# Optimization experiments

Measured on AMD Instinct MI355X. Metric: run time of the kernel, lower is better.

The kernel has to match this reference:

```python
import jax, jax.numpy as jnp
import numpy as np

K = 512        # num_embeddings
D = 64         # embedding_dim
BETA = 0.25
B, S = 64, 4096


def setup_inputs() -> dict:
    key = jax.random.key(0)
    k1, k2 = jax.random.split(key)
    latents = jax.random.normal(k1, (B, S, D), dtype=jnp.float32)
    # torch init: uniform_(-1/K, 1/K)
    embedding = jax.random.uniform(k2, (K, D), dtype=jnp.float32,
                                   minval=-1.0 / K, maxval=1.0 / K)
    return {"latents": latents, "embedding": embedding}


def reference(latents, embedding):
    d = embedding.shape[1]
    flat = latents.reshape(-1, d)                       # [N, D]
    # squared-euclidean distances via norm expansion: [N, K]
    dist = (jnp.sum(flat * flat, axis=1, keepdims=True)
            + jnp.sum(embedding * embedding, axis=1)
            - 2.0 * flat @ embedding.T)
    inds = jnp.argmin(dist, axis=1)                     # [N] (channel = identity)
    # one-hot @ codebook == gather; same math, no [N,K] one-hot materialized
    quantized = embedding[inds].reshape(latents.shape)  # [B, S, D]
    commitment_loss = jnp.mean((jax.lax.stop_gradient(quantized) - latents) ** 2)
    embedding_loss = jnp.mean((quantized - jax.lax.stop_gradient(latents)) ** 2)
    vq_loss = commitment_loss * BETA + embedding_loss
    # straight-through estimator
    quantized_st = latents + jax.lax.stop_gradient(quantized - latents)
    return quantized_st, vq_loss
```

## Files before the change

kernel.cpp:

```cpp
#include <hip/hip_runtime.h>
#include <math.h>
#include <stdint.h>

#define KCODES 512
#define DIM 64
#define NROWS (64 * 4096)
#define BLOCK 512
#define ROWS_PER_WAVE 16
#define BM ((BLOCK / 64) * ROWS_PER_WAVE)
#define NBLK (NROWS / BM)

typedef float f32x4 __attribute__((ext_vector_type(4)));
typedef long long i64t;

typedef __attribute__((address_space(3))) uint32_t* lds_ptr_t;
typedef const __attribute__((address_space(1))) uint32_t* glb_ptr_t;

__global__ void vq_prep_kernel(const float* __restrict__ emb,
                               float* __restrict__ en512,
                               uint8_t* __restrict__ ebf8) {
    int k = blockIdx.x * blockDim.x + threadIdx.x;
    if (k >= KCODES) return;
    const float4* e4 = reinterpret_cast<const float4*>(emb + k * DIM);
    float s0 = 0.f, s1 = 0.f, s2 = 0.f, s3 = 0.f;
#pragma unroll
    for (int j = 0; j < 8; ++j) {
        float4 v0 = e4[j * 2];
        float4 v1 = e4[j * 2 + 1];
        s0 = fmaf(v0.x, v0.x, s0); s1 = fmaf(v0.y, v0.y, s1);
        s2 = fmaf(v0.z, v0.z, s2); s3 = fmaf(v0.w, v0.w, s3);
        s0 = fmaf(v1.x, v1.x, s0); s1 = fmaf(v1.y, v1.y, s1);
        s2 = fmaf(v1.z, v1.z, s2); s3 = fmaf(v1.w, v1.w, s3);
        uint32_t lo = 0, hi = 0;
        lo = __builtin_amdgcn_cvt_pk_fp8_f32(-1024.f * v0.x, -1024.f * v0.y, lo, false);
        lo = __builtin_amdgcn_cvt_pk_fp8_f32(-1024.f * v0.z, -1024.f * v0.w, lo, true);
        hi = __builtin_amdgcn_cvt_pk_fp8_f32(-1024.f * v1.x, -1024.f * v1.y, hi, false);
        hi = __builtin_amdgcn_cvt_pk_fp8_f32(-1024.f * v1.z, -1024.f * v1.w, hi, true);
        uint2 p; p.x = lo; p.y = hi;
        *reinterpret_cast<uint2*>(&ebf8[k * DIM + ((j ^ (k & 7)) << 3)]) = p;
    }
    en512[k] = 512.f * (1.0f + (s0 + s1) + (s2 + s3));
}

__launch_bounds__(BLOCK, 8)
__global__ void vq_mfma_kernel(const float* __restrict__ lat,
                               const float* __restrict__ emb,
                               const float* __restrict__ en512,
                               const uint8_t* __restrict__ ebf8,
                               float* __restrict__ outq,
                               float* __restrict__ partials) {
    __shared__ __align__(16) uint8_t e_lds[KCODES * DIM];
    __shared__ float en_lds[KCODES];
    __shared__ float wsum_lds[BLOCK / 64];

    const int t = threadIdx.x;
    const int lane = t & 63, wid = t >> 6;
    const int l15 = lane & 15, lq = lane >> 4;
    const int swz = l15 & 7;

    const uint32_t bid = (blockIdx.x & 7) * (NBLK / 8) + (blockIdx.x >> 3);
    const uint32_t waverow = bid * BM + (uint32_t)wid * ROWS_PER_WAVE;

#pragma unroll
    for (int i = 0; i < 4; ++i) {
        int c = t + i * BLOCK;
        __builtin_amdgcn_global_load_lds(
            (glb_ptr_t)(const void*)(ebf8 + c * 16),
            (lds_ptr_t)(void*)(&e_lds[c * 16]), 16, 0, 0);
    }

    float4 araw[2][2];
#pragma unroll
    for (int ks = 0; ks < 2; ++ks) {
        const float* xp = lat + (waverow + l15) * DIM + ks * 32 + lq * 8;
        araw[ks][0] = reinterpret_cast<const float4*>(xp)[0];
        araw[ks][1] = reinterpret_cast<const float4*>(xp)[1];
    }
    en_lds[t] = en512[t];
    __syncthreads();

    float xsq = 0.f, lsum = 0.f;
    i64t afrag[2];
#pragma unroll
    for (int ks = 0; ks < 2; ++ks) {
        float4 v0 = araw[ks][0], v1 = araw[ks][1];
        xsq = fmaf(v0.x, v0.x, xsq); xsq = fmaf(v0.y, v0.y, xsq);
        xsq = fmaf(v0.z, v0.z, xsq); xsq = fmaf(v0.w, v0.w, xsq);
        xsq = fmaf(v1.x, v1.x, xsq); xsq = fmaf(v1.y, v1.y, xsq);
        xsq = fmaf(v1.z, v1.z, xsq); xsq = fmaf(v1.w, v1.w, xsq);
        uint32_t lo = 0, hi = 0;
        lo = __builtin_amdgcn_cvt_pk_fp8_f32(v0.x, v0.y, lo, false);
        lo = __builtin_amdgcn_cvt_pk_fp8_f32(v0.z, v0.w, lo, true);
        hi = __builtin_amdgcn_cvt_pk_fp8_f32(v1.x, v1.y, hi, false);
        hi = __builtin_amdgcn_cvt_pk_fp8_f32(v1.z, v1.w, hi, true);
        afrag[ks] = (i64t)(((uint64_t)hi << 32) | (uint64_t)lo);
    }

    uint32_t best[4];
#pragma unroll
    for (int r = 0; r < 4; ++r) best[r] = 0xFFFFFFFFu;

#pragma unroll 4
    for (int nf = 0; nf < 32; ++nf) {
        const int n = nf * 16 + l15;
        i64t b0 = *reinterpret_cast<const i64t*>(
            &e_lds[n * DIM + ((lq ^ swz) << 3)]);
        i64t b1 = *reinterpret_cast<const i64t*>(
            &e_lds[n * DIM + (((lq + 4) ^ swz) << 3)]);
        float en = en_lds[n];
        f32x4 acc = {en, en, en, en};
        acc = __builtin_amdgcn_mfma_f32_16x16x32_fp8_fp8(afrag[0], b0, acc, 0, 0, 0);
        acc = __builtin_amdgcn_mfma_f32_16x16x32_fp8_fp8(afrag[1], b1, acc, 0, 0, 0);
        const uint32_t nn = (uint32_t)n;
#pragma unroll
        for (int r = 0; r < 4; ++r) {
            uint32_t k = (__float_as_uint(acc[r]) & 0xFFFFFE00u) | nn;
            best[r] = min(best[r], k);
        }
    }

#pragma unroll
    for (int off = 1; off < 16; off <<= 1) {
#pragma unroll
        for (int r = 0; r < 4; ++r) {
            uint32_t o = (uint32_t)__shfl_xor((int)best[r], off, 64);
            best[r] = min(best[r], o);
        }
    }

    if (l15 == 0) {
#pragma unroll
        for (int r = 0; r < 4; ++r)
            lsum = fmaf(__uint_as_float(best[r] & 0xFFFFFE00u),
                        (1.f / 512.f), lsum - 1.0f);
    }

    const float4* emb4 = reinterpret_cast<const float4*>(emb);
    float4* out4 = reinterpret_cast<float4*>(outq);
#pragma unroll
    for (int r = 0; r < 4; ++r) {
        const uint32_t k = best[r] & 511u;
        const uint32_t grow = waverow + lq * 4 + r;
        float4 e4 = emb4[k * 16 + l15];
        out4[grow * 16 + l15] = e4;
    }

    lsum += xsq;

#pragma unroll
    for (int off = 32; off > 0; off >>= 1)
        lsum += __shfl_down(lsum, off, 64);
    if (lane == 0) wsum_lds[wid] = lsum;
    __syncthreads();
    if (t == 0) {
        float s = 0.f;
#pragma unroll
        for (int w = 0; w < BLOCK / 64; ++w) s += wsum_lds[w];
        partials[blockIdx.x] = s;
    }
}

__global__ void vq_loss_kernel(const float* __restrict__ partials,
                               float* __restrict__ loss) {
    float s = 0.f;
    for (int i = threadIdx.x; i < NBLK; i += 256) s += partials[i];
#pragma unroll
    for (int off = 32; off > 0; off >>= 1)
        s += __shfl_down(s, off, 64);
    __shared__ float wsum[4];
    const int lane = threadIdx.x & 63;
    const int wid = threadIdx.x >> 6;
    if (lane == 0) wsum[wid] = s;
    __syncthreads();
    if (threadIdx.x == 0) {
        float tsum = 0.f;
#pragma unroll
        for (int w = 0; w < 4; ++w) tsum += wsum[w];
        loss[0] = 1.25f * (tsum / (float)((size_t)NROWS * DIM));
    }
}

extern "C" void kernel_launch(void* const* d_in, const int* in_sizes, int n_in,
                              void* d_out, int out_size, void* d_ws, size_t ws_size,
                              hipStream_t stream) {
    const float* lat = (const float*)d_in[0];
    const float* emb = (const float*)d_in[1];
    float* outq = (float*)d_out;
    float* loss = (float*)d_out + (size_t)NROWS * DIM;

    float* en512 = (float*)d_ws;
    uint8_t* ebf8 = (uint8_t*)d_ws + 2048;
    float* partials = (float*)((char*)d_ws + 34816);

    vq_prep_kernel<<<2, 256, 0, stream>>>(emb, en512, ebf8);
    vq_mfma_kernel<<<NBLK, BLOCK, 0, stream>>>(lat, emb, en512, ebf8, outq, partials);
    vq_loss_kernel<<<1, 256, 0, stream>>>(partials, loss);
}
```

Baseline: 41.03 us.

## Process two row chunks per block, prefetching the next chunk's latents during scoring

Each block now handles two consecutive 128-row chunks. It issues the second chunk's latent loads right after converting the first chunk, so the global load overlaps the MFMA scoring loop. This also halves the grid and amortises the 32KB codebook LDS fill over twice the rows. Latent loads and quantized stores now use nontemporal hints. The costs are fewer blocks to hide latency and more registers held across the scoring loop.

```diff
diff --git a/kernel.cpp b/kernel.cpp
--- a/kernel.cpp
+++ b/kernel.cpp
@@ -8,7 +8,8 @@
 #define BLOCK 512
 #define ROWS_PER_WAVE 16
 #define BM ((BLOCK / 64) * ROWS_PER_WAVE)
-#define NBLK (NROWS / BM)
+#define CHUNKS 2
+#define NBLK (NROWS / (BM * CHUNKS))
 
 typedef float f32x4 __attribute__((ext_vector_type(4)));
 typedef long long i64t;
@@ -59,7 +60,7 @@
     const int swz = l15 & 7;
 
     const uint32_t bid = (blockIdx.x & 7) * (NBLK / 8) + (blockIdx.x >> 3);
-    const uint32_t waverow = bid * BM + (uint32_t)wid * ROWS_PER_WAVE;
+    const uint32_t blockrow = bid * (BM * CHUNKS);
 
 #pragma unroll
     for (int i = 0; i < 4; ++i) {
@@ -69,81 +70,103 @@
             (lds_ptr_t)(void*)(&e_lds[c * 16]), 16, 0, 0);
     }
 
-    float4 araw[2][2];
-#pragma unroll
-    for (int ks = 0; ks < 2; ++ks) {
-        const float* xp = lat + (waverow + l15) * DIM + ks * 32 + lq * 8;
-        araw[ks][0] = reinterpret_cast<const float4*>(xp)[0];
-        araw[ks][1] = reinterpret_cast<const float4*>(xp)[1];
-    }
+    f32x4 araw[2][2];
+    auto load_a = [&](int c) {
+        const uint32_t rowbase = blockrow + (uint32_t)c * BM +
+                                 (uint32_t)wid * ROWS_PER_WAVE;
+#pragma unroll
+        for (int ks = 0; ks < 2; ++ks) {
+            const float* xp = lat + (rowbase + l15) * DIM + ks * 32 + lq * 8;
+            araw[ks][0] = __builtin_nontemporal_load(
+                reinterpret_cast<const f32x4*>(xp));
+            araw[ks][1] = __builtin_nontemporal_load(
+                reinterpret_cast<const f32x4*>(xp) + 1);
+        }
+    };
+
+    load_a(0);
     en_lds[t] = en512[t];
     __syncthreads();
 
     float xsq = 0.f, lsum = 0.f;
     i64t afrag[2];
-#pragma unroll
-    for (int ks = 0; ks < 2; ++ks) {
-        float4 v0 = araw[ks][0], v1 = araw[ks][1];
-        xsq = fmaf(v0.x, v0.x, xsq); xsq = fmaf(v0.y, v0.y, xsq);
-        xsq = fmaf(v0.z, v0.z, xsq); xsq = fmaf(v0.w, v0.w, xsq);
-        xsq = fmaf(v1.x, v1.x, xsq); xsq = fmaf(v1.y, v1.y, xsq);
-        xsq = fmaf(v1.z, v1.z, xsq); xsq = fmaf(v1.w, v1.w, xsq);
-        uint32_t lo = 0, hi = 0;
-        lo = __builtin_amdgcn_cvt_pk_fp8_f32(v0.x, v0.y, lo, false);
-        lo = __builtin_amdgcn_cvt_pk_fp8_f32(v0.z, v0.w, lo, true);
-        hi = __builtin_amdgcn_cvt_pk_fp8_f32(v1.x, v1.y, hi, false);
-        hi = __builtin_amdgcn_cvt_pk_fp8_f32(v1.z, v1.w, hi, true);
-        afrag[ks] = (i64t)(((uint64_t)hi << 32) | (uint64_t)lo);
-    }
-
     uint32_t best[4];
-#pragma unroll
-    for (int r = 0; r < 4; ++r) best[r] = 0xFFFFFFFFu;
-
+
+    auto cvt_a = [&]() {
+#pragma unroll
+        for (int ks = 0; ks < 2; ++ks) {
+            f32x4 v0 = araw[ks][0], v1 = araw[ks][1];
+            xsq = fmaf(v0[0], v0[0], xsq); xsq = fmaf(v0[1], v0[1], xsq);
+            xsq = fmaf(v0[2], v0[2], xsq); xsq = fmaf(v0[3], v0[3], xsq);
+            xsq = fmaf(v1[0], v1[0], xsq); xsq = fmaf(v1[1], v1[1], xsq);
+            xsq = fmaf(v1[2], v1[2], xsq); xsq = fmaf(v1[3], v1[3], xsq);
+            uint32_t lo = 0, hi = 0;
+            lo = __builtin_amdgcn_cvt_pk_fp8_f32(v0[0], v0[1], lo, false);
+            lo = __builtin_amdgcn_cvt_pk_fp8_f32(v0[2], v0[3], lo, true);
+            hi = __builtin_amdgcn_cvt_pk_fp8_f32(v1[0], v1[1], hi, false);
+            hi = __builtin_amdgcn_cvt_pk_fp8_f32(v1[2], v1[3], hi, true);
+            afrag[ks] = (i64t)(((uint64_t)hi << 32) | (uint64_t)lo);
+        }
+    };
+
+    auto score = [&]() {
+#pragma unroll
+        for (int r = 0; r < 4; ++r) best[r] = 0xFFFFFFFFu;
 #pragma unroll 4
-    for (int nf = 0; nf < 32; ++nf) {
-        const int n = nf * 16 + l15;
-        i64t b0 = *reinterpret_cast<const i64t*>(
-            &e_lds[n * DIM + ((lq ^ swz) << 3)]);
-        i64t b1 = *reinterpret_cast<const i64t*>(
-            &e_lds[n * DIM + (((lq + 4) ^ swz) << 3)]);
-        float en = en_lds[n];
-        f32x4 acc = {en, en, en, en};
-        acc = __builtin_amdgcn_mfma_f32_16x16x32_fp8_fp8(afrag[0], b0, acc, 0, 0, 0);
-        acc = __builtin_amdgcn_mfma_f32_16x16x32_fp8_fp8(afrag[1], b1, acc, 0, 0, 0);
-        const uint32_t nn = (uint32_t)n;
+        for (int nf = 0; nf < 32; ++nf) {
+            const int n = nf * 16 + l15;
+            i64t b0 = *reinterpret_cast<const i64t*>(
+                &e_lds[n * DIM + ((lq ^ swz) << 3)]);
+            i64t b1 = *reinterpret_cast<const i64t*>(
+                &e_lds[n * DIM + (((lq + 4) ^ swz) << 3)]);
+            float en = en_lds[n];
+            f32x4 acc = {en, en, en, en};
+            acc = __builtin_amdgcn_mfma_f32_16x16x32_fp8_fp8(afrag[0], b0, acc, 0, 0, 0);
+            acc = __builtin_amdgcn_mfma_f32_16x16x32_fp8_fp8(afrag[1], b1, acc, 0, 0, 0);
+            const uint32_t nn = (uint32_t)n;
+#pragma unroll
+            for (int r = 0; r < 4; ++r) {
+                uint32_t k = (__float_as_uint(acc[r]) & 0xFFFFFE00u) | nn;
+                best[r] = min(best[r], k);
+            }
+        }
+    };
+
+    auto finish = [&](int c) {
+#pragma unroll
+        for (int off = 1; off < 16; off <<= 1) {
+#pragma unroll
+            for (int r = 0; r < 4; ++r) {
+                uint32_t o = (uint32_t)__shfl_xor((int)best[r], off, 64);
+                best[r] = min(best[r], o);
+            }
+        }
+        if (l15 == 0) {
+#pragma unroll
+            for (int r = 0; r < 4; ++r)
+                lsum = fmaf(__uint_as_float(best[r] & 0xFFFFFE00u),
+                            (1.f / 512.f), lsum - 1.0f);
+        }
+        const uint32_t rowbase = blockrow + (uint32_t)c * BM +
+                                 (uint32_t)wid * ROWS_PER_WAVE;
+        const f32x4* emb4 = reinterpret_cast<const f32x4*>(emb);
+        f32x4* out4 = reinterpret_cast<f32x4*>(outq);
 #pragma unroll
         for (int r = 0; r < 4; ++r) {
-            uint32_t k = (__float_as_uint(acc[r]) & 0xFFFFFE00u) | nn;
-            best[r] = min(best[r], k);
-        }
-    }
-
-#pragma unroll
-    for (int off = 1; off < 16; off <<= 1) {
-#pragma unroll
-        for (int r = 0; r < 4; ++r) {
-            uint32_t o = (uint32_t)__shfl_xor((int)best[r], off, 64);
-            best[r] = min(best[r], o);
-        }
-    }
-
-    if (l15 == 0) {
-#pragma unroll
-        for (int r = 0; r < 4; ++r)
-            lsum = fmaf(__uint_as_float(best[r] & 0xFFFFFE00u),
-                        (1.f / 512.f), lsum - 1.0f);
-    }
-
-    const float4* emb4 = reinterpret_cast<const float4*>(emb);
-    float4* out4 = reinterpret_cast<float4*>(outq);
-#pragma unroll
-    for (int r = 0; r < 4; ++r) {
-        const uint32_t k = best[r] & 511u;
-        const uint32_t grow = waverow + lq * 4 + r;
-        float4 e4 = emb4[k * 16 + l15];
-        out4[grow * 16 + l15] = e4;
-    }
+            const uint32_t k = best[r] & 511u;
+            const uint32_t grow = rowbase + lq * 4 + r;
+            f32x4 e4 = emb4[k * 16 + l15];
+            __builtin_nontemporal_store(e4, &out4[grow * 16 + l15]);
+        }
+    };
+
+    cvt_a();
+    load_a(1);
+    score();
+    finish(0);
+    cvt_a();
+    score();
+    finish(1);
 
     lsum += xsq;
 
```

Measured after the change: 55.24 us. 34.6% more time.

## Hold FP8 codebook in registers and stream latent rows per persistent wave

Applied to the files above, without the earlier changes.

The fused distance/argmin kernel becomes a persistent-style kernel with 512 blocks of 256 threads. Each wave loads the whole FP8 codebook into registers once as MFMA A operands, then loops over 128 latent rows with double-buffered global loads, treating the latents as the B operand. This removes the per-block LDS codebook copy and the per-fragment LDS reads. Argmin now keeps per-lane packed keys and needs only two cross-lane shuffles. The cost is very high register pressure (64 i64 codebook fragments per lane) and much lower occupancy, which may limit how well memory latency is hidden.

```diff
diff --git a/kernel.cpp b/kernel.cpp
--- a/kernel.cpp
+++ b/kernel.cpp
@@ -5,16 +5,12 @@
 #define KCODES 512
 #define DIM 64
 #define NROWS (64 * 4096)
-#define BLOCK 512
-#define ROWS_PER_WAVE 16
-#define BM ((BLOCK / 64) * ROWS_PER_WAVE)
-#define NBLK (NROWS / BM)
+#define BLOCK 256
+#define NBLK 512
+#define ROWS_PER_WAVE 128
 
 typedef float f32x4 __attribute__((ext_vector_type(4)));
 typedef long long i64t;
-
-typedef __attribute__((address_space(3))) uint32_t* lds_ptr_t;
-typedef const __attribute__((address_space(1))) uint32_t* glb_ptr_t;
 
 __global__ void vq_prep_kernel(const float* __restrict__ emb,
                                float* __restrict__ en512,
@@ -37,112 +33,119 @@
         hi = __builtin_amdgcn_cvt_pk_fp8_f32(-1024.f * v1.x, -1024.f * v1.y, hi, false);
         hi = __builtin_amdgcn_cvt_pk_fp8_f32(-1024.f * v1.z, -1024.f * v1.w, hi, true);
         uint2 p; p.x = lo; p.y = hi;
-        *reinterpret_cast<uint2*>(&ebf8[k * DIM + ((j ^ (k & 7)) << 3)]) = p;
+        *reinterpret_cast<uint2*>(&ebf8[k * DIM + (j << 3)]) = p;
     }
     en512[k] = 512.f * (1.0f + (s0 + s1) + (s2 + s3));
 }
 
-__launch_bounds__(BLOCK, 8)
-__global__ void vq_mfma_kernel(const float* __restrict__ lat,
-                               const float* __restrict__ emb,
-                               const float* __restrict__ en512,
-                               const uint8_t* __restrict__ ebf8,
-                               float* __restrict__ outq,
-                               float* __restrict__ partials) {
-    __shared__ __align__(16) uint8_t e_lds[KCODES * DIM];
+__launch_bounds__(BLOCK, 2)
+__global__ void vq_stream_kernel(const float* __restrict__ lat,
+                                 const float* __restrict__ emb,
+                                 const float* __restrict__ en512,
+                                 const uint8_t* __restrict__ ebf8,
+                                 float* __restrict__ outq,
+                                 float* __restrict__ partials) {
     __shared__ float en_lds[KCODES];
     __shared__ float wsum_lds[BLOCK / 64];
 
     const int t = threadIdx.x;
     const int lane = t & 63, wid = t >> 6;
     const int l15 = lane & 15, lq = lane >> 4;
-    const int swz = l15 & 7;
-
-    const uint32_t bid = (blockIdx.x & 7) * (NBLK / 8) + (blockIdx.x >> 3);
-    const uint32_t waverow = bid * BM + (uint32_t)wid * ROWS_PER_WAVE;
-
-#pragma unroll
-    for (int i = 0; i < 4; ++i) {
-        int c = t + i * BLOCK;
-        __builtin_amdgcn_global_load_lds(
-            (glb_ptr_t)(const void*)(ebf8 + c * 16),
-            (lds_ptr_t)(void*)(&e_lds[c * 16]), 16, 0, 0);
-    }
-
-    float4 araw[2][2];
-#pragma unroll
-    for (int ks = 0; ks < 2; ++ks) {
-        const float* xp = lat + (waverow + l15) * DIM + ks * 32 + lq * 8;
-        araw[ks][0] = reinterpret_cast<const float4*>(xp)[0];
-        araw[ks][1] = reinterpret_cast<const float4*>(xp)[1];
-    }
+    const uint32_t wrow = ((uint32_t)blockIdx.x * (BLOCK / 64) + wid) * ROWS_PER_WAVE;
+
     en_lds[t] = en512[t];
+    en_lds[t + BLOCK] = en512[t + BLOCK];
+
+    i64t acode[32][2];
+#pragma unroll
+    for (int nf = 0; nf < 32; ++nf) {
+#pragma unroll
+        for (int ks = 0; ks < 2; ++ks) {
+            acode[nf][ks] = *reinterpret_cast<const i64t*>(
+                ebf8 + (uint32_t)(nf * 16 + l15) * DIM + ks * 32 + lq * 8);
+        }
+    }
     __syncthreads();
 
     float xsq = 0.f, lsum = 0.f;
-    i64t afrag[2];
-#pragma unroll
-    for (int ks = 0; ks < 2; ++ks) {
-        float4 v0 = araw[ks][0], v1 = araw[ks][1];
-        xsq = fmaf(v0.x, v0.x, xsq); xsq = fmaf(v0.y, v0.y, xsq);
-        xsq = fmaf(v0.z, v0.z, xsq); xsq = fmaf(v0.w, v0.w, xsq);
-        xsq = fmaf(v1.x, v1.x, xsq); xsq = fmaf(v1.y, v1.y, xsq);
-        xsq = fmaf(v1.z, v1.z, xsq); xsq = fmaf(v1.w, v1.w, xsq);
-        uint32_t lo = 0, hi = 0;
-        lo = __builtin_amdgcn_cvt_pk_fp8_f32(v0.x, v0.y, lo, false);
-        lo = __builtin_amdgcn_cvt_pk_fp8_f32(v0.z, v0.w, lo, true);
-        hi = __builtin_amdgcn_cvt_pk_fp8_f32(v1.x, v1.y, hi, false);
-        hi = __builtin_amdgcn_cvt_pk_fp8_f32(v1.z, v1.w, hi, true);
-        afrag[ks] = (i64t)(((uint64_t)hi << 32) | (uint64_t)lo);
-    }
-
-    uint32_t best[4];
-#pragma unroll
-    for (int r = 0; r < 4; ++r) best[r] = 0xFFFFFFFFu;
-
-#pragma unroll 4
-    for (int nf = 0; nf < 32; ++nf) {
-        const int n = nf * 16 + l15;
-        i64t b0 = *reinterpret_cast<const i64t*>(
-            &e_lds[n * DIM + ((lq ^ swz) << 3)]);
-        i64t b1 = *reinterpret_cast<const i64t*>(
-            &e_lds[n * DIM + (((lq + 4) ^ swz) << 3)]);
-        float en = en_lds[n];
-        f32x4 acc = {en, en, en, en};
-        acc = __builtin_amdgcn_mfma_f32_16x16x32_fp8_fp8(afrag[0], b0, acc, 0, 0, 0);
-        acc = __builtin_amdgcn_mfma_f32_16x16x32_fp8_fp8(afrag[1], b1, acc, 0, 0, 0);
-        const uint32_t nn = (uint32_t)n;
+    const f32x4* emb4 = reinterpret_cast<const f32x4*>(emb);
+    f32x4* out4 = reinterpret_cast<f32x4*>(outq);
+
+    float4 brA[2][2], brB[2][2];
+
+    auto load_b = [&](float4 (&br)[2][2], uint32_t row0) {
+#pragma unroll
+        for (int ks = 0; ks < 2; ++ks) {
+            const float* xp = lat + (row0 + l15) * DIM + ks * 32 + lq * 8;
+            br[ks][0] = reinterpret_cast<const float4*>(xp)[0];
+            br[ks][1] = reinterpret_cast<const float4*>(xp)[1];
+        }
+    };
+
+    auto process = [&](float4 (&br)[2][2], uint32_t row0) {
+        i64t bfrag[2];
+#pragma unroll
+        for (int ks = 0; ks < 2; ++ks) {
+            float4 v0 = br[ks][0], v1 = br[ks][1];
+            xsq = fmaf(v0.x, v0.x, xsq); xsq = fmaf(v0.y, v0.y, xsq);
+            xsq = fmaf(v0.z, v0.z, xsq); xsq = fmaf(v0.w, v0.w, xsq);
+            xsq = fmaf(v1.x, v1.x, xsq); xsq = fmaf(v1.y, v1.y, xsq);
+            xsq = fmaf(v1.z, v1.z, xsq); xsq = fmaf(v1.w, v1.w, xsq);
+            uint32_t lo = 0, hi = 0;
+            lo = __builtin_amdgcn_cvt_pk_fp8_f32(v0.x, v0.y, lo, false);
+            lo = __builtin_amdgcn_cvt_pk_fp8_f32(v0.z, v0.w, lo, true);
+            hi = __builtin_amdgcn_cvt_pk_fp8_f32(v1.x, v1.y, hi, false);
+            hi = __builtin_amdgcn_cvt_pk_fp8_f32(v1.z, v1.w, hi, true);
+            bfrag[ks] = (i64t)(((uint64_t)hi << 32) | (uint64_t)lo);
+        }
+
+        uint32_t kb[4];
+#pragma unroll
+        for (int r = 0; r < 4; ++r) kb[r] = 0xFFFFFFFFu;
+
+#pragma unroll
+        for (int nf = 0; nf < 32; ++nf) {
+            f32x4 acc = {0.f, 0.f, 0.f, 0.f};
+            acc = __builtin_amdgcn_mfma_f32_16x16x32_fp8_fp8(acode[nf][0], bfrag[0], acc, 0, 0, 0);
+            acc = __builtin_amdgcn_mfma_f32_16x16x32_fp8_fp8(acode[nf][1], bfrag[1], acc, 0, 0, 0);
+            f32x4 en4 = *reinterpret_cast<const f32x4*>(&en_lds[nf * 16 + lq * 4]);
+#pragma unroll
+            for (int r = 0; r < 4; ++r) {
+                float s = acc[r] + en4[r];
+                uint32_t key = (__float_as_uint(s) & 0xFFFFFE00u) | (uint32_t)nf;
+                kb[r] = min(kb[r], key);
+            }
+        }
+
+        uint32_t full = 0xFFFFFFFFu;
 #pragma unroll
         for (int r = 0; r < 4; ++r) {
-            uint32_t k = (__float_as_uint(acc[r]) & 0xFFFFFE00u) | nn;
-            best[r] = min(best[r], k);
-        }
-    }
-
-#pragma unroll
-    for (int off = 1; off < 16; off <<= 1) {
-#pragma unroll
-        for (int r = 0; r < 4; ++r) {
-            uint32_t o = (uint32_t)__shfl_xor((int)best[r], off, 64);
-            best[r] = min(best[r], o);
-        }
-    }
-
-    if (l15 == 0) {
-#pragma unroll
-        for (int r = 0; r < 4; ++r)
-            lsum = fmaf(__uint_as_float(best[r] & 0xFFFFFE00u),
-                        (1.f / 512.f), lsum - 1.0f);
-    }
-
-    const float4* emb4 = reinterpret_cast<const float4*>(emb);
-    float4* out4 = reinterpret_cast<float4*>(outq);
-#pragma unroll
-    for (int r = 0; r < 4; ++r) {
-        const uint32_t k = best[r] & 511u;
-        const uint32_t grow = waverow + lq * 4 + r;
-        float4 e4 = emb4[k * 16 + l15];
-        out4[grow * 16 + l15] = e4;
+            uint32_t code = (kb[r] & 31u) * 16u + (uint32_t)(lq * 4 + r);
+            uint32_t fk = (kb[r] & 0xFFFFFE00u) | code;
+            full = min(full, fk);
+        }
+        full = min(full, (uint32_t)__shfl_xor((int)full, 16, 64));
+        full = min(full, (uint32_t)__shfl_xor((int)full, 32, 64));
+
+        if (lq == 0)
+            lsum += __uint_as_float(full & 0xFFFFFE00u) * (1.f / 512.f) - 1.0f;
+
+        const uint32_t k = full & 511u;
+        const uint32_t rbase = (row0 + l15) * 16;
+#pragma unroll
+        for (int i = 0; i < 4; ++i) {
+            const int ch = lq + i * 4;
+            out4[rbase + ch] = emb4[k * 16 + ch];
+        }
+    };
+
+    load_b(brA, wrow);
+    for (uint32_t cc = 0; cc < 4; ++cc) {
+        const uint32_t r0 = wrow + cc * 32;
+        load_b(brB, r0 + 16);
+        process(brA, r0);
+        if (cc < 3) load_b(brA, r0 + 32);
+        process(brB, r0 + 16);
     }
 
     lsum += xsq;
@@ -193,6 +196,6 @@
     float* partials = (float*)((char*)d_ws + 34816);
 
     vq_prep_kernel<<<2, 256, 0, stream>>>(emb, en512, ebf8);
-    vq_mfma_kernel<<<NBLK, BLOCK, 0, stream>>>(lat, emb, en512, ebf8, outq, partials);
+    vq_stream_kernel<<<NBLK, BLOCK, 0, stream>>>(lat, emb, en512, ebf8, outq, partials);
     vq_loss_kernel<<<1, 256, 0, stream>>>(partials, loss);
 }
```

Result: slower. 103.4 us (+151.9%).
